# Optimization experiments

Measured on AMD Instinct MI355X. Metric: run time of the kernel, lower is better.

The kernel has to match this reference:

```python
import jax, jax.numpy as jnp
import numpy as np

B, D_IN, H0, H1, LAT, C = 8192, 2048, 1024, 512, 128, 8
SCALE = 0.02  # weight init scale to keep activations well-conditioned


def _unshared_linear_relu(x, labels, W, b):
    """Per-cluster Linear+ReLU routing. x:[B,din], W:[C,din,dout], b:[C,dout].
    Computes all cluster branches then selects per-row branch (same math as
    torch's mask gather->Linear->scatter; rows never reorder)."""
    y = jax.nn.relu(jnp.einsum('bi,cio->bco', x, W) + b[None, :, :])  # [B,C,dout]
    return jnp.take_along_axis(y, labels[:, None, None], axis=1)[:, 0, :]


def setup_inputs() -> dict:
    key = jax.random.key(0)
    ks = jax.random.split(key, 12)
    return {
        'x': jax.random.normal(ks[0], (B, D_IN), dtype=jnp.float32),
        'cluster_labels': jax.random.randint(ks[1], (B,), 0, C, dtype=jnp.int32),
        'eps': jax.random.normal(ks[2], (B, LAT), dtype=jnp.float32),
        'W_enc0': jax.random.normal(ks[3], (C, D_IN, H0), dtype=jnp.float32) * SCALE,
        'b_enc0': jnp.zeros((C, H0), dtype=jnp.float32),
        'W_enc1': jax.random.normal(ks[4], (H0, H1), dtype=jnp.float32) * SCALE,
        'b_enc1': jnp.zeros((H1,), dtype=jnp.float32),
        'W_mu': jax.random.normal(ks[5], (H1, LAT), dtype=jnp.float32) * SCALE,
        'b_mu': jnp.zeros((LAT,), dtype=jnp.float32),
        'W_logvar': jax.random.normal(ks[6], (H1, LAT), dtype=jnp.float32) * SCALE,
        'b_logvar': jnp.zeros((LAT,), dtype=jnp.float32),
        'W_dec0': jax.random.normal(ks[7], (LAT, H1), dtype=jnp.float32) * SCALE,
        'b_dec0': jnp.zeros((H1,), dtype=jnp.float32),
        'W_dec1': jax.random.normal(ks[8], (C, H1, H0), dtype=jnp.float32) * SCALE,
        'b_dec1': jnp.zeros((C, H0), dtype=jnp.float32),
        'W_out': jax.random.normal(ks[9], (H0, D_IN), dtype=jnp.float32) * SCALE,
        'b_out': jnp.zeros((D_IN,), dtype=jnp.float32),
    }


def reference(x, cluster_labels, eps,
              W_enc0, b_enc0, W_enc1, b_enc1,
              W_mu, b_mu, W_logvar, b_logvar,
              W_dec0, b_dec0, W_dec1, b_dec1,
              W_out, b_out):
    labels = cluster_labels.astype(jnp.int32)
    # encoder: unshared layer 0, shared layer 1
    h = _unshared_linear_relu(x, labels, W_enc0, b_enc0)          # [B, H0]
    h = jax.nn.relu(h @ W_enc1 + b_enc1)                          # [B, H1]
    # shared latent heads
    mu = h @ W_mu + b_mu                                          # [B, LAT]
    logvar = h @ W_logvar + b_logvar                              # [B, LAT]
    # reparameterize
    z = mu + eps * jnp.exp(0.5 * logvar)                          # [B, LAT]
    # decoder: shared layer 0, unshared layer 1 (hidden_dims reversed)
    d = jax.nn.relu(z @ W_dec0 + b_dec0)                          # [B, H1]
    d = _unshared_linear_relu(d, labels, W_dec1, b_dec1)          # [B, H0]
    # shared output layer (no activation)
    recon = d @ W_out + b_out                                     # [B, D_IN]
    return recon, mu, logvar
```

## Files before the change

### kernel.cpp

```cpp
#include <hip/hip_runtime.h>


#define DEVI __device__ __forceinline__

constexpr int B_    = 8192;
constexpr int DIN   = 2048;
constexpr int H0_   = 1024;
constexpr int H1_   = 512;
constexpr int LAT_  = 128;
constexpr int NC    = 8;

constexpr int BM = 128, BN = 128, BK = 32;
constexpr int TCAP   = 72;
constexpr int BP_CAP = TCAP * BM;

#define MI_NTILES 8
#define MI_TILEC  16

typedef __attribute__((ext_vector_type(8))) short bf16x8;
typedef __attribute__((ext_vector_type(4))) float f32x4;

#define LDS_BARRIER() asm volatile("s_waitcnt lgkmcnt(0)\n\ts_barrier" ::: "memory")

DEVI unsigned short f2bf(float f) {
  union { float f; unsigned u; } a; a.f = f;
  unsigned r = a.u + 0x7fffu + ((a.u >> 16) & 1u);
  return (unsigned short)(r >> 16);
}

constexpr size_t AL256(size_t x) { return (x + 255) & ~(size_t)255; }
constexpr size_t OFF_META = 0;
constexpr size_t OFF_PERM = 512;
constexpr size_t OFF_XG   = AL256(OFF_PERM + (size_t)BP_CAP * 4);
constexpr size_t OFF_H0   = AL256(OFF_XG  + (size_t)BP_CAP * DIN * 2);
constexpr size_t OFF_H1   = AL256(OFF_H0  + (size_t)BP_CAP * H0_ * 2);
constexpr size_t OFF_MLP  = AL256(OFF_H1  + (size_t)BP_CAP * H1_ * 2);
constexpr size_t OFF_BML  = AL256(OFF_MLP + (size_t)BP_CAP * 256 * 4);
constexpr size_t OFF_WT0  = AL256(OFF_BML + 256 * 4);
constexpr size_t OFF_WT1  = AL256(OFF_WT0 + (size_t)NC * DIN * H0_ * 2);
constexpr size_t OFF_WML  = AL256(OFF_WT1 + (size_t)H0_ * H1_ * 2);
constexpr size_t OFF_WD0  = AL256(OFF_WML + (size_t)256 * H1_ * 2);
constexpr size_t OFF_WD1  = AL256(OFF_WD0 + (size_t)LAT_ * H1_ * 2);
constexpr size_t OFF_WOUT = AL256(OFF_WD1 + (size_t)NC * H1_ * H0_ * 2);

__global__ void setup_all(const int* __restrict__ labels, int* __restrict__ meta,
                          int* __restrict__ perm, const float* __restrict__ b_mu,
                          const float* __restrict__ b_lv, float* __restrict__ b_ml) {
  __shared__ int cnt[NC], base[NC];
  int t = threadIdx.x;
  if (t < NC) cnt[t] = 0;
  if (t < 256) b_ml[t] = (t < 128) ? b_mu[t] : b_lv[t - 128];
  __syncthreads();
  for (int i = t; i < B_; i += 1024) atomicAdd(&cnt[labels[i]], 1);
  for (int i = t; i < BP_CAP; i += 1024) perm[i] = -1;
  __syncthreads();
  if (t == 0) {
    int off = 0, nt = 0;
    for (int c = 0; c < NC; ++c) {
      base[c] = off;
      int k = (cnt[c] + BM - 1) >> 7;
      for (int j = 0; j < k; ++j) meta[MI_TILEC + nt + j] = c;
      nt += k;
      off += k << 7;
    }
    meta[MI_NTILES] = nt;
  }
  __syncthreads();
  if (t < NC) cnt[t] = base[t];
  __syncthreads();
  for (int i = t; i < B_; i += 1024) {
    int pos = atomicAdd(&cnt[labels[i]], 1);
    perm[pos] = i;
  }
}

struct SegDesc { const float* src; unsigned short* dst; int K, N, nb, tstart; };
struct SegTable { SegDesc s[7]; };

__global__ void convert_all(SegTable t) {
  __shared__ float tl[64][33];
  int tile = blockIdx.x;
  int si = 0;
#pragma unroll
  for (int i = 1; i < 7; ++i) si += (tile >= t.s[i].tstart) ? 1 : 0;
  const SegDesc sd = t.s[si];
  int local = tile - sd.tstart;
  int tpb = (sd.K >> 6) * (sd.N >> 5);
  int b = local / tpb, rem = local - b * tpb;
  int tk = rem / (sd.N >> 5), tn = rem - tk * (sd.N >> 5);
  const float* s = sd.src + (size_t)b * sd.K * sd.N;
  unsigned short* d = sd.dst + (size_t)b * sd.K * sd.N;
  int n0 = tn * 32, k0 = tk * 64;
  int tx = threadIdx.x, ty = threadIdx.y;
  for (int i = ty; i < 64; i += 8)
    tl[i][tx] = s[(size_t)(k0 + i) * sd.N + n0 + tx];
  __syncthreads();
  int id = ty * 32 + tx;
  int j = id >> 3;
  int kk = (id & 7) * 8;
  unsigned short v[8];
#pragma unroll
  for (int q = 0; q < 8; ++q) v[q] = f2bf(tl[kk + q][j]);
  *(int4*)&d[(size_t)(n0 + j) * sd.K + k0 + kk] = *(int4*)v;
}

__global__ void gather_x_kernel(const float* __restrict__ x, const int* __restrict__ perm,
                                unsigned short* __restrict__ xg) {
  int p = blockIdx.x;
  int c4 = blockIdx.y * 256 + threadIdx.x;
  int src = perm[p];
  float4 v = make_float4(0.f, 0.f, 0.f, 0.f);
  if (src >= 0) v = ((const float4*)(x + (size_t)src * DIN))[c4];
  ushort4 o;
  o.x = f2bf(v.x); o.y = f2bf(v.y); o.z = f2bf(v.z); o.w = f2bf(v.w);
  ((ushort4*)(xg + (size_t)p * DIN))[c4] = o;
}

__global__ void z_kernel(const float* __restrict__ mlp, const float* __restrict__ eps,
                         const int* __restrict__ perm, unsigned short* __restrict__ z,
                         float* __restrict__ out_mu, float* __restrict__ out_lv) {
  int p = blockIdx.x, j = threadIdx.x;
  int src = perm[p];
  float zz = 0.f;
  if (src >= 0) {
    float m = mlp[(size_t)p * 256 + j];
    float l = mlp[(size_t)p * 256 + 128 + j];
    zz = m + eps[(size_t)src * LAT_ + j] * expf(0.5f * l);
    out_mu[(size_t)src * LAT_ + j] = m;
    out_lv[(size_t)src * LAT_ + j] = l;
  }
  z[(size_t)p * LAT_ + j] = f2bf(zz);
}

template <int OUT_MODE, bool RELU, bool PCW, bool PCB>
__global__ __launch_bounds__(256, 2)
void gemm_kernel(const unsigned short* __restrict__ A,
                 const unsigned short* __restrict__ Bt,
                 const float* __restrict__ bias,
                 void* __restrict__ Cout,
                 const int* __restrict__ meta,
                 const int* __restrict__ perm,
                 int K, int N, int ldc) {
  const int ntn = N >> 7;
  const int sup = 8 * ntn;
  const int gid = blockIdx.x;
  const int tm  = (gid / sup) * 8 + (gid & 7);
  const int tn  = (gid % sup) >> 3;
  if (tm >= meta[MI_NTILES]) return;

  int cluster = 0;
  if (PCW || PCB) cluster = meta[MI_TILEC + tm];
  const unsigned short* Bp = Bt + (PCW ? (size_t)cluster * (size_t)N * K : 0);
  const float* bb = bias + (PCB ? (size_t)cluster * N : 0);

  __shared__ alignas(16) unsigned short As[2][BM * BK];
  __shared__ alignas(16) unsigned short Bs[2][BN * BK];

  const int tid  = threadIdx.x;
  const int w    = tid >> 6, lane = tid & 63;
  const int fr   = lane & 15, quad = lane >> 4;
  const int wm   = (w >> 1) * 64, wn = (w & 1) * 64;

  const int s0 = (w * 2 + 0) * 64 + lane;
  const int s1 = (w * 2 + 1) * 64 + lane;
  const int r0 = s0 >> 2, r1 = s1 >> 2;
  const int c0 = (s0 & 3) ^ ((r0 >> 1) & 3);
  const int c1 = (s1 & 3) ^ ((r1 >> 1) & 3);
  const size_t aoff0 = (size_t)(tm * BM + r0) * K + c0 * 8;
  const size_t aoff1 = (size_t)(tm * BM + r1) * K + c1 * 8;
  const size_t boff0 = (size_t)(tn * BN + r0) * K + c0 * 8;
  const size_t boff1 = (size_t)(tn * BN + r1) * K + c1 * 8;
  const int l0 = s0 * 8, l1 = s1 * 8;

  int aro[4], bro[4];
#pragma unroll
  for (int i = 0; i < 4; ++i) {
    int R = wm + i * 16 + fr;
    aro[i] = (R * 4 + (quad ^ ((R >> 1) & 3))) * 8;
    R = wn + i * 16 + fr;
    bro[i] = (R * 4 + (quad ^ ((R >> 1) & 3))) * 8;
  }

  f32x4 acc[4][4] = {};

  int4 ra0 = *(const int4*)(A  + aoff0);
  int4 ra1 = *(const int4*)(A  + aoff1);
  int4 rb0 = *(const int4*)(Bp + boff0);
  int4 rb1 = *(const int4*)(Bp + boff1);
  *(int4*)&As[0][l0] = ra0;
  *(int4*)&As[0][l1] = ra1;
  *(int4*)&Bs[0][l0] = rb0;
  *(int4*)&Bs[0][l1] = rb1;
  if (K > BK) {
    ra0 = *(const int4*)(A  + aoff0 + BK);
    ra1 = *(const int4*)(A  + aoff1 + BK);
    rb0 = *(const int4*)(Bp + boff0 + BK);
    rb1 = *(const int4*)(Bp + boff1 + BK);
  }
  LDS_BARRIER();

  int cur = 0;
  for (int k0 = BK; k0 < K; k0 += BK) {
    const int nxt = cur ^ 1;
    bf16x8 af[4], bfr[4];
#pragma unroll
    for (int i = 0; i < 4; ++i) af[i]  = *(const bf16x8*)&As[cur][aro[i]];
#pragma unroll
    for (int i = 0; i < 4; ++i) bfr[i] = *(const bf16x8*)&Bs[cur][bro[i]];
#pragma unroll
    for (int mi = 0; mi < 4; ++mi)
#pragma unroll
      for (int ni = 0; ni < 4; ++ni)
        acc[mi][ni] = __builtin_amdgcn_mfma_f32_16x16x32_bf16(af[mi], bfr[ni], acc[mi][ni], 0, 0, 0);

    *(int4*)&As[nxt][l0] = ra0;
    *(int4*)&As[nxt][l1] = ra1;
    *(int4*)&Bs[nxt][l0] = rb0;
    *(int4*)&Bs[nxt][l1] = rb1;
    if (k0 + BK < K) {
      ra0 = *(const int4*)(A  + aoff0 + k0 + BK);
      ra1 = *(const int4*)(A  + aoff1 + k0 + BK);
      rb0 = *(const int4*)(Bp + boff0 + k0 + BK);
      rb1 = *(const int4*)(Bp + boff1 + k0 + BK);
    }
    LDS_BARRIER();
    cur = nxt;
  }

  {
    bf16x8 af[4], bfr[4];
#pragma unroll
    for (int i = 0; i < 4; ++i) af[i]  = *(const bf16x8*)&As[cur][aro[i]];
#pragma unroll
    for (int i = 0; i < 4; ++i) bfr[i] = *(const bf16x8*)&Bs[cur][bro[i]];
#pragma unroll
    for (int mi = 0; mi < 4; ++mi)
#pragma unroll
      for (int ni = 0; ni < 4; ++ni)
        acc[mi][ni] = __builtin_amdgcn_mfma_f32_16x16x32_bf16(af[mi], bfr[ni], acc[mi][ni], 0, 0, 0);
  }

  float bv[4];
#pragma unroll
  for (int ni = 0; ni < 4; ++ni) bv[ni] = bb[tn * BN + wn + ni * 16 + fr];

#pragma unroll
  for (int mi = 0; mi < 4; ++mi) {
#pragma unroll
    for (int r = 0; r < 4; ++r) {
      int m = tm * BM + wm + mi * 16 + quad * 4 + r;
      int orow = m;
      if (OUT_MODE == 2) orow = perm[m];
#pragma unroll
      for (int ni = 0; ni < 4; ++ni) {
        int n = tn * BN + wn + ni * 16 + fr;
        float v = acc[mi][ni][r] + bv[ni];
        if (RELU) v = fmaxf(v, 0.f);
        if (OUT_MODE == 0) {
          ((unsigned short*)Cout)[(size_t)m * N + n] = f2bf(v);
        } else if (OUT_MODE == 1) {
          ((float*)Cout)[(size_t)m * N + n] = v;
        } else {
          if (orow >= 0) ((float*)Cout)[(size_t)orow * ldc + n] = v;
        }
      }
    }
  }
}

extern "C" void kernel_launch(void* const* d_in, const int* in_sizes, int n_in,
                              void* d_out, int out_size, void* d_ws, size_t ws_size,
                              hipStream_t stream) {
  const float* x        = (const float*)d_in[0];
  const int*   labels   = (const int*)d_in[1];
  const float* eps      = (const float*)d_in[2];
  const float* W_enc0   = (const float*)d_in[3];
  const float* b_enc0   = (const float*)d_in[4];
  const float* W_enc1   = (const float*)d_in[5];
  const float* b_enc1   = (const float*)d_in[6];
  const float* W_mu     = (const float*)d_in[7];
  const float* b_mu     = (const float*)d_in[8];
  const float* W_logvar = (const float*)d_in[9];
  const float* b_logvar = (const float*)d_in[10];
  const float* W_dec0   = (const float*)d_in[11];
  const float* b_dec0   = (const float*)d_in[12];
  const float* W_dec1   = (const float*)d_in[13];
  const float* b_dec1   = (const float*)d_in[14];
  const float* W_out    = (const float*)d_in[15];
  const float* b_out    = (const float*)d_in[16];

  float* out_recon = (float*)d_out;
  float* out_mu    = out_recon + (size_t)B_ * DIN;
  float* out_lv    = out_mu + (size_t)B_ * LAT_;

  char* ws = (char*)d_ws;
  int* meta            = (int*)(ws + OFF_META);
  int* perm            = (int*)(ws + OFF_PERM);
  unsigned short* xg   = (unsigned short*)(ws + OFF_XG);
  unsigned short* h0   = (unsigned short*)(ws + OFF_H0);
  unsigned short* h1   = (unsigned short*)(ws + OFF_H1);
  float* mlp           = (float*)(ws + OFF_MLP);
  float* b_ml          = (float*)(ws + OFF_BML);
  unsigned short* Wt0  = (unsigned short*)(ws + OFF_WT0);
  unsigned short* Wt1  = (unsigned short*)(ws + OFF_WT1);
  unsigned short* Wml  = (unsigned short*)(ws + OFF_WML);
  unsigned short* Wd0  = (unsigned short*)(ws + OFF_WD0);
  unsigned short* Wd1  = (unsigned short*)(ws + OFF_WD1);
  unsigned short* Wout = (unsigned short*)(ws + OFF_WOUT);
  unsigned short* d1 = xg;
  unsigned short* d0 = h0;
  unsigned short* z  = h1;

  SegTable st;
  int ts = 0;
  auto seg = [&](int i, const float* s, unsigned short* d, int K, int N, int nb) {
    st.s[i] = SegDesc{s, d, K, N, nb, ts};
    ts += (K / 64) * (N / 32) * nb;
  };
  seg(0, W_enc0,   Wt0,                      DIN,  H0_,  NC);
  seg(1, W_enc1,   Wt1,                      H0_,  H1_,  1);
  seg(2, W_mu,     Wml,                      H1_,  LAT_, 1);
  seg(3, W_logvar, Wml + (size_t)LAT_ * H1_, H1_,  LAT_, 1);
  seg(4, W_dec0,   Wd0,                      LAT_, H1_,  1);
  seg(5, W_dec1,   Wd1,                      H1_,  H0_,  NC);
  seg(6, W_out,    Wout,                     H0_,  DIN,  1);

  setup_all<<<1, 1024, 0, stream>>>(labels, meta, perm, b_mu, b_logvar, b_ml);
  convert_all<<<ts, dim3(32, 8), 0, stream>>>(st);
  gather_x_kernel<<<dim3(BP_CAP, DIN / (256 * 4)), 256, 0, stream>>>(x, perm, xg);

  gemm_kernel<0, true, true, true><<<TCAP * (H0_ / BN), 256, 0, stream>>>(
      xg, Wt0, b_enc0, h0, meta, perm, DIN, H0_, 0);
  gemm_kernel<0, true, false, false><<<TCAP * (H1_ / BN), 256, 0, stream>>>(
      h0, Wt1, b_enc1, h1, meta, perm, H0_, H1_, 0);
  gemm_kernel<1, false, false, false><<<TCAP * (256 / BN), 256, 0, stream>>>(
      h1, Wml, b_ml, mlp, meta, perm, H1_, 256, 0);
  z_kernel<<<BP_CAP, 128, 0, stream>>>(mlp, eps, perm, z, out_mu, out_lv);
  gemm_kernel<0, true, false, false><<<TCAP * (H1_ / BN), 256, 0, stream>>>(
      z, Wd0, b_dec0, d0, meta, perm, LAT_, H1_, 0);
  gemm_kernel<0, true, true, true><<<TCAP * (H0_ / BN), 256, 0, stream>>>(
      d0, Wd1, b_dec1, d1, meta, perm, H1_, H0_, 0);
  gemm_kernel<2, false, false, false><<<TCAP * (DIN / BN), 256, 0, stream>>>(
      d1, Wout, b_out, out_recon, meta, perm, H0_, DIN, DIN);

  (void)in_sizes; (void)n_in; (void)out_size; (void)ws_size;
}
```

Baseline: 434.7 us.

## Use direct global-to-LDS loads and 2-wave 128x64-per-wave GEMM tiles

```diff
diff --git a/kernel.cpp b/kernel.cpp
--- a/kernel.cpp
+++ b/kernel.cpp
@@ -20,12 +20,17 @@
 typedef __attribute__((ext_vector_type(8))) short bf16x8;
 typedef __attribute__((ext_vector_type(4))) float f32x4;
 
-#define LDS_BARRIER() asm volatile("s_waitcnt lgkmcnt(0)\n\ts_barrier" ::: "memory")
-
 DEVI unsigned short f2bf(float f) {
   union { float f; unsigned u; } a; a.f = f;
   unsigned r = a.u + 0x7fffu + ((a.u >> 16) & 1u);
   return (unsigned short)(r >> 16);
+}
+
+DEVI void glds16(const unsigned short* g, unsigned short* l) {
+  __builtin_amdgcn_global_load_lds(
+      (const __attribute__((address_space(1))) unsigned int*)g,
+      (__attribute__((address_space(3))) unsigned int*)l,
+      16, 0, 0);
 }
 
 constexpr size_t AL256(size_t x) { return (x + 255) & ~(size_t)255; }
@@ -133,7 +138,7 @@
 }
 
 template <int OUT_MODE, bool RELU, bool PCW, bool PCB>
-__global__ __launch_bounds__(256, 2)
+__global__ __launch_bounds__(128, 2)
 void gemm_kernel(const unsigned short* __restrict__ A,
                  const unsigned short* __restrict__ Bt,
                  const float* __restrict__ bias,
@@ -159,101 +164,79 @@
   const int tid  = threadIdx.x;
   const int w    = tid >> 6, lane = tid & 63;
   const int fr   = lane & 15, quad = lane >> 4;
-  const int wm   = (w >> 1) * 64, wn = (w & 1) * 64;
-
-  const int s0 = (w * 2 + 0) * 64 + lane;
-  const int s1 = (w * 2 + 1) * 64 + lane;
-  const int r0 = s0 >> 2, r1 = s1 >> 2;
-  const int c0 = (s0 & 3) ^ ((r0 >> 1) & 3);
-  const int c1 = (s1 & 3) ^ ((r1 >> 1) & 3);
-  const size_t aoff0 = (size_t)(tm * BM + r0) * K + c0 * 8;
-  const size_t aoff1 = (size_t)(tm * BM + r1) * K + c1 * 8;
-  const size_t boff0 = (size_t)(tn * BN + r0) * K + c0 * 8;
-  const size_t boff1 = (size_t)(tn * BN + r1) * K + c1 * 8;
-  const int l0 = s0 * 8, l1 = s1 * 8;
-
-  int aro[4], bro[4];
+
+  const unsigned short* aP[4];
+  const unsigned short* bP[4];
+#pragma unroll
+  for (int j = 0; j < 4; ++j) {
+    int s = (w * 4 + j) * 64 + lane;
+    int r = s >> 2;
+    int c = (s & 3) ^ ((r >> 1) & 3);
+    aP[j] = A  + (size_t)(tm * BM + r) * K + c * 8;
+    bP[j] = Bp + (size_t)(tn * BN + r) * K + c * 8;
+  }
+
+  int aro[8], bro[4];
+#pragma unroll
+  for (int i = 0; i < 8; ++i) {
+    int R = i * 16 + fr;
+    aro[i] = (R * 4 + (quad ^ ((R >> 1) & 3))) * 8;
+  }
 #pragma unroll
   for (int i = 0; i < 4; ++i) {
-    int R = wm + i * 16 + fr;
-    aro[i] = (R * 4 + (quad ^ ((R >> 1) & 3))) * 8;
-    R = wn + i * 16 + fr;
+    int R = w * 64 + i * 16 + fr;
     bro[i] = (R * 4 + (quad ^ ((R >> 1) & 3))) * 8;
   }
 
-  f32x4 acc[4][4] = {};
-
-  int4 ra0 = *(const int4*)(A  + aoff0);
-  int4 ra1 = *(const int4*)(A  + aoff1);
-  int4 rb0 = *(const int4*)(Bp + boff0);
-  int4 rb1 = *(const int4*)(Bp + boff1);
-  *(int4*)&As[0][l0] = ra0;
-  *(int4*)&As[0][l1] = ra1;
-  *(int4*)&Bs[0][l0] = rb0;
-  *(int4*)&Bs[0][l1] = rb1;
-  if (K > BK) {
-    ra0 = *(const int4*)(A  + aoff0 + BK);
-    ra1 = *(const int4*)(A  + aoff1 + BK);
-    rb0 = *(const int4*)(Bp + boff0 + BK);
-    rb1 = *(const int4*)(Bp + boff1 + BK);
-  }
-  LDS_BARRIER();
+  f32x4 acc[8][4] = {};
+
+  auto stage = [&](int buf, int k0) {
+#pragma unroll
+    for (int j = 0; j < 4; ++j) {
+      glds16(aP[j] + k0, &As[buf][(w * 4 + j) * 512]);
+      glds16(bP[j] + k0, &Bs[buf][(w * 4 + j) * 512]);
+    }
+  };
+
+  auto compute = [&](int buf) {
+    bf16x8 af[8], bfr[4];
+#pragma unroll
+    for (int i = 0; i < 4; ++i) bfr[i] = *(const bf16x8*)&Bs[buf][bro[i]];
+#pragma unroll
+    for (int i = 0; i < 8; ++i) af[i]  = *(const bf16x8*)&As[buf][aro[i]];
+#pragma unroll
+    for (int mi = 0; mi < 8; ++mi)
+#pragma unroll
+      for (int ni = 0; ni < 4; ++ni)
+        acc[mi][ni] = __builtin_amdgcn_mfma_f32_16x16x32_bf16(af[mi], bfr[ni], acc[mi][ni], 0, 0, 0);
+  };
+
+  stage(0, 0);
+  __syncthreads();
 
   int cur = 0;
   for (int k0 = BK; k0 < K; k0 += BK) {
-    const int nxt = cur ^ 1;
-    bf16x8 af[4], bfr[4];
-#pragma unroll
-    for (int i = 0; i < 4; ++i) af[i]  = *(const bf16x8*)&As[cur][aro[i]];
-#pragma unroll
-    for (int i = 0; i < 4; ++i) bfr[i] = *(const bf16x8*)&Bs[cur][bro[i]];
-#pragma unroll
-    for (int mi = 0; mi < 4; ++mi)
-#pragma unroll
-      for (int ni = 0; ni < 4; ++ni)
-        acc[mi][ni] = __builtin_amdgcn_mfma_f32_16x16x32_bf16(af[mi], bfr[ni], acc[mi][ni], 0, 0, 0);
-
-    *(int4*)&As[nxt][l0] = ra0;
-    *(int4*)&As[nxt][l1] = ra1;
-    *(int4*)&Bs[nxt][l0] = rb0;
-    *(int4*)&Bs[nxt][l1] = rb1;
-    if (k0 + BK < K) {
-      ra0 = *(const int4*)(A  + aoff0 + k0 + BK);
-      ra1 = *(const int4*)(A  + aoff1 + k0 + BK);
-      rb0 = *(const int4*)(Bp + boff0 + k0 + BK);
-      rb1 = *(const int4*)(Bp + boff1 + k0 + BK);
-    }
-    LDS_BARRIER();
-    cur = nxt;
-  }
-
-  {
-    bf16x8 af[4], bfr[4];
-#pragma unroll
-    for (int i = 0; i < 4; ++i) af[i]  = *(const bf16x8*)&As[cur][aro[i]];
-#pragma unroll
-    for (int i = 0; i < 4; ++i) bfr[i] = *(const bf16x8*)&Bs[cur][bro[i]];
-#pragma unroll
-    for (int mi = 0; mi < 4; ++mi)
-#pragma unroll
-      for (int ni = 0; ni < 4; ++ni)
-        acc[mi][ni] = __builtin_amdgcn_mfma_f32_16x16x32_bf16(af[mi], bfr[ni], acc[mi][ni], 0, 0, 0);
-  }
+    stage(cur ^ 1, k0);
+    compute(cur);
+    __syncthreads();
+    cur ^= 1;
+  }
+  compute(cur);
 
   float bv[4];
 #pragma unroll
-  for (int ni = 0; ni < 4; ++ni) bv[ni] = bb[tn * BN + wn + ni * 16 + fr];
-
-#pragma unroll
-  for (int mi = 0; mi < 4; ++mi) {
+  for (int ni = 0; ni < 4; ++ni) bv[ni] = bb[tn * BN + w * 64 + ni * 16 + fr];
+
+#pragma unroll
+  for (int mi = 0; mi < 8; ++mi) {
 #pragma unroll
     for (int r = 0; r < 4; ++r) {
-      int m = tm * BM + wm + mi * 16 + quad * 4 + r;
+      int m = tm * BM + mi * 16 + quad * 4 + r;
       int orow = m;
       if (OUT_MODE == 2) orow = perm[m];
 #pragma unroll
       for (int ni = 0; ni < 4; ++ni) {
-        int n = tn * BN + wn + ni * 16 + fr;
+        int n = tn * BN + w * 64 + ni * 16 + fr;
         float v = acc[mi][ni][r] + bv[ni];
         if (RELU) v = fmaxf(v, 0.f);
         if (OUT_MODE == 0) {
@@ -329,18 +312,18 @@
   convert_all<<<ts, dim3(32, 8), 0, stream>>>(st);
   gather_x_kernel<<<dim3(BP_CAP, DIN / (256 * 4)), 256, 0, stream>>>(x, perm, xg);
 
-  gemm_kernel<0, true, true, true><<<TCAP * (H0_ / BN), 256, 0, stream>>>(
+  gemm_kernel<0, true, true, true><<<TCAP * (H0_ / BN), 128, 0, stream>>>(
       xg, Wt0, b_enc0, h0, meta, perm, DIN, H0_, 0);
-  gemm_kernel<0, true, false, false><<<TCAP * (H1_ / BN), 256, 0, stream>>>(
+  gemm_kernel<0, true, false, false><<<TCAP * (H1_ / BN), 128, 0, stream>>>(
       h0, Wt1, b_enc1, h1, meta, perm, H0_, H1_, 0);
-  gemm_kernel<1, false, false, false><<<TCAP * (256 / BN), 256, 0, stream>>>(
+  gemm_kernel<1, false, false, false><<<TCAP * (256 / BN), 128, 0, stream>>>(
       h1, Wml, b_ml, mlp, meta, perm, H1_, 256, 0);
   z_kernel<<<BP_CAP, 128, 0, stream>>>(mlp, eps, perm, z, out_mu, out_lv);
-  gemm_kernel<0, true, false, false><<<TCAP * (H1_ / BN), 256, 0, stream>>>(
+  gemm_kernel<0, true, false, false><<<TCAP * (H1_ / BN), 128, 0, stream>>>(
       z, Wd0, b_dec0, d0, meta, perm, LAT_, H1_, 0);
-  gemm_kernel<0, true, true, true><<<TCAP * (H0_ / BN), 256, 0, stream>>>(
+  gemm_kernel<0, true, true, true><<<TCAP * (H0_ / BN), 128, 0, stream>>>(
       d0, Wd1, b_dec1, d1, meta, perm, H1_, H0_, 0);
-  gemm_kernel<2, false, false, false><<<TCAP * (DIN / BN), 256, 0, stream>>>(
+  gemm_kernel<2, false, false, false><<<TCAP * (DIN / BN), 128, 0, stream>>>(
       d1, Wout, b_out, out_recon, meta, perm, H0_, DIN, DIN);
 
   (void)in_sizes; (void)n_in; (void)out_size; (void)ws_size;
```

Result: slower. 509.9 us (+17.3%).
